# Kernel tuning notes

Hardware: AMD Instinct MI355X
Metric: run time of the kernel (lower is better)

Reference implementation:

```python
import jax, jax.numpy as jnp
import numpy as np

B = 256          # number of trees
DEPTH = 8        # complete binary tree depth -> 9 levels
M = 2 ** (DEPTH + 1) - 1   # 511 nodes per tree
N = B * M        # 130816 total nodes
X_SIZE = 128
H_SIZE = 128


def _build_forest():
    j = np.arange(M)
    parent_local = np.maximum((j - 1) // 2, 0)
    lvl = np.array([int(x + 1).bit_length() - 1 for x in j], dtype=np.int32)
    off = (np.arange(B) * M).astype(np.int32)
    parent = (parent_local[None, :] + off[:, None]).reshape(-1).astype(np.int32)
    level = np.tile(lvl, B)
    tree_id = np.repeat(np.arange(B, dtype=np.int32), M)
    isleaf = (level == DEPTH)
    jj = j[1:]
    edge_src = (jj[None, :] + off[:, None]).reshape(-1).astype(np.int32)   # child
    edge_dst = parent[edge_src]                                            # parent
    return parent, level, tree_id, isleaf, edge_src, edge_dst, off


def setup_inputs() -> dict:
    key = jax.random.key(0)
    ks = jax.random.split(key, 12)
    _, level, tree_id, isleaf, edge_src, edge_dst, root_ids = _build_forest()
    sx = 1.0 / np.sqrt(X_SIZE)
    sh = 1.0 / np.sqrt(H_SIZE)
    sxh = 1.0 / np.sqrt(X_SIZE + H_SIZE)
    inp = {
        "X": jax.random.normal(ks[0], (N, X_SIZE), dtype=jnp.float32),
        "h0": jnp.zeros((N, H_SIZE), jnp.float32),
        "c0": jnp.zeros((N, H_SIZE), jnp.float32),
        # bottom-up cell params
        "W_iou_bu": jax.random.normal(ks[1], (3 * H_SIZE, X_SIZE), dtype=jnp.float32) * sx,
        "U_iou_bu": jax.random.normal(ks[2], (3 * H_SIZE, H_SIZE), dtype=jnp.float32) * sh,
        "b_iou_bu": jnp.zeros((1, 3 * H_SIZE), jnp.float32),
        "Uf_bu": jax.random.normal(ks[3], (H_SIZE, H_SIZE), dtype=jnp.float32) * sh,
        "bf_bu": jax.random.normal(ks[4], (H_SIZE,), dtype=jnp.float32) * sh,
        # top-down cell params (x_size = X_SIZE + H_SIZE)
        "W_iou_td": jax.random.normal(ks[5], (3 * H_SIZE, X_SIZE + H_SIZE), dtype=jnp.float32) * sxh,
        "U_iou_td": jax.random.normal(ks[6], (3 * H_SIZE, H_SIZE), dtype=jnp.float32) * sh,
        "b_iou_td": jnp.zeros((1, 3 * H_SIZE), jnp.float32),
        "Uf_td": jax.random.normal(ks[7], (H_SIZE, H_SIZE), dtype=jnp.float32) * sh,
        "bf_td": jax.random.normal(ks[8], (H_SIZE,), dtype=jnp.float32) * sh,
        # graph structure
        "edge_src": jnp.asarray(edge_src),
        "edge_dst": jnp.asarray(edge_dst),
        "level": jnp.asarray(level),
        "tree_id": jnp.asarray(tree_id),
        "isleaf": jnp.asarray(isleaf),
        "root_ids": jnp.asarray(root_ids),
    }
    return inp


def _propagate(X_in, W_iou, U_iou, b_iou, Uf, bf, src, dst, level, no_in, h0, c0, order):
    """Level-synchronous ChildSum TreeLSTM propagation (== dgl.prop_nodes_topo)."""
    n = X_in.shape[0]
    WX = X_in @ W_iou.T                                   # [N, 3H]
    h, c = h0, c0
    for t in order:
        h_src = h[src]                                    # [E, H] gather child/parent states
        c_src = c[src]
        h_tild = jax.ops.segment_sum(h_src, dst, num_segments=n)
        f = jax.nn.sigmoid(h_src @ Uf.T + bf)             # per-edge forget gate
        c_red = jax.ops.segment_sum(f * c_src, dst, num_segments=n)
        iou = WX + h_tild @ U_iou.T + b_iou
        i, o, u = jnp.split(iou, 3, axis=1)
        c_base = jnp.where(no_in[:, None], c0, c_red)     # frontier nodes with no in-edges keep init c
        c_new = jax.nn.sigmoid(i) * jnp.tanh(u) + c_base
        h_new = jax.nn.sigmoid(o) * jnp.tanh(c_new)
        m = (level == t)[:, None]                          # only commit current topological level
        h = jnp.where(m, h_new, h)
        c = jnp.where(m, c_new, c)
    return h


def reference(X, h0, c0, W_iou_bu, U_iou_bu, b_iou_bu, Uf_bu, bf_bu,
              W_iou_td, U_iou_td, b_iou_td, Uf_td, bf_td,
              edge_src, edge_dst, level, tree_id, isleaf, root_ids):
    # bottom-up: messages flow child -> parent, leaves first
    h_bu = _propagate(X, W_iou_bu, U_iou_bu, b_iou_bu, Uf_bu, bf_bu,
                      edge_src, edge_dst, level, isleaf, h0, c0,
                      order=range(DEPTH, -1, -1))
    # top-down: reversed edges, root first
    X_td = jnp.concatenate([X, h_bu], axis=1)
    h_td = _propagate(X_td, W_iou_td, U_iou_td, b_iou_td, Uf_td, bf_td,
                      edge_dst, edge_src, level, level == 0, h0, c0,
                      order=range(0, DEPTH + 1))
    root_h_bottom_up = h_bu[root_ids]                     # [B, H]
    leaf = isleaf.astype(h_td.dtype)
    sums = jax.ops.segment_sum(h_td * leaf[:, None], tree_id, num_segments=root_ids.shape[0])
    cnt = jax.ops.segment_sum(leaf, tree_id, num_segments=root_ids.shape[0])
    leaves_h_top_down = sums / cnt[:, None]               # per-tree mean over leaves
    return jnp.concatenate([root_h_bottom_up, leaves_h_top_down], axis=1)
```

## Files before the change

### kernel.cpp

```cpp
#include <hip/hip_runtime.h>
#include <cmath>

#define NTREE 256
#define MPT 511
#define NNODE (NTREE * MPT)
#define HS 128

typedef __bf16 bf16x8 __attribute__((ext_vector_type(8)));
typedef float  f32x4  __attribute__((ext_vector_type(4)));

__device__ __forceinline__ float sigf(float x) {
  float e = __builtin_amdgcn_exp2f(x * -1.44269504f);
  return __builtin_amdgcn_rcpf(1.0f + e);
}
__device__ __forceinline__ float tanh_fast(float x) {
  float e = __builtin_amdgcn_exp2f(x * -2.88539008f);
  return __builtin_amdgcn_rcpf(1.0f + e) * 2.0f - 1.0f;
}
__device__ __forceinline__ f32x4 mm(bf16x8 a, bf16x8 b, f32x4 c) {
  return __builtin_amdgcn_mfma_f32_16x16x32_bf16(a, b, c, 0, 0, 0);
}
__device__ __forceinline__ int swz(int row, int rb, int kb) { return row * rb + (kb ^ ((row & 7) << 4)); }
__device__ __forceinline__ void st8(char* s, int row, int rb, int chunk, bf16x8 v) {
  *reinterpret_cast<bf16x8*>(s + swz(row, rb, chunk * 16)) = v;
}
__device__ __forceinline__ bf16x8 ld8(const char* s, int row, int rb, int kb) {
  return *reinterpret_cast<const bf16x8*>(s + swz(row, rb, kb));
}
__device__ __forceinline__ bf16x8 g8(const __bf16* p) { return *reinterpret_cast<const bf16x8*>(p); }
__device__ __forceinline__ bf16x8 gx8(const float* p) {
  float4 v0 = reinterpret_cast<const float4*>(p)[0];
  float4 v1 = reinterpret_cast<const float4*>(p)[1];
  bf16x8 o;
  o[0] = (__bf16)v0.x; o[1] = (__bf16)v0.y; o[2] = (__bf16)v0.z; o[3] = (__bf16)v0.w;
  o[4] = (__bf16)v1.x; o[5] = (__bf16)v1.y; o[6] = (__bf16)v1.z; o[7] = (__bf16)v1.w;
  return o;
}
__device__ __forceinline__ void stbf(char* s, int row, int rb, int kbyte, float v) {
  *reinterpret_cast<__bf16*>(s + row * rb + (kbyte ^ ((row & 7) << 4))) = (__bf16)v;
}

template <int MODE, bool EPI>
__global__ void __launch_bounds__(256, 2)
level_big(int t,
          const float*  __restrict__ Xf,
          const __bf16* __restrict__ W,
          const float*  __restrict__ bp,
          const __bf16* __restrict__ Uf,
          const float*  __restrict__ bf_,
          __bf16* __restrict__ h_bu,
          __bf16* __restrict__ h_td,
          float*  __restrict__ cws,
          float*  __restrict__ part)
{
  constexpr int KA = (MODE == 0) ? 128 : (MODE == 1) ? 256 : 384;
  constexpr int KS = KA / 32;
  constexpr int BK = (MODE == 3) ? 384 : 256;
  constexpr int RB = KA * 2;
  constexpr int HB = (MODE == 0) ? 0 : (MODE == 1) ? 256 : 512;
  constexpr bool LEAFOUT = (MODE == 3 && !EPI);

  __shared__ __align__(16) char sA[64 * RB];
  __shared__ int sG[64], sP[64];

  const int tid = threadIdx.x;
  const int w = tid >> 6, l = tid & 63, lr = l & 15, lk = l >> 4;

  if (tid < 64) {
    int v = blockIdx.x * 64 + tid;
    int b = v >> t;
    int j = (1 << t) - 1 + (v & ((1 << t) - 1));
    sG[tid] = b * MPT + j;
    sP[tid] = b * MPT + ((j - 1) >> 1);
  }
  __syncthreads();

#pragma unroll
  for (int it = 0; it < 4; ++it) {
    int idx = tid + it * 256, n = idx >> 4, e = idx & 15;
    st8(sA, n, RB, e, gx8(Xf + (size_t)sG[n] * HS + e * 8));
  }
  if constexpr (MODE >= 1) {
#pragma unroll
    for (int it = 0; it < 4; ++it) {
      int idx = tid + it * 256, n = idx >> 4, e = idx & 15;
      st8(sA, n, RB, 16 + e, g8(h_bu + (size_t)sG[n] * HS + e * 8));
    }
  }
  if constexpr (MODE == 3) {
#pragma unroll
    for (int it = 0; it < 4; ++it) {
      int idx = tid + it * 256, n = idx >> 4, e = idx & 15;
      st8(sA, n, RB, 32 + e, g8(h_td + (size_t)sP[n] * HS + e * 8));
    }
  }
  __syncthreads();

  float cb[2][4][4];
  float bia[2], boa[2], bua[2], bfa[2];
#pragma unroll
  for (int nf = 0; nf < 2; ++nf) {
    const int ch = w * 32 + nf * 16 + lr;
    bia[nf] = bp[ch]; boa[nf] = bp[ch + 128]; bua[nf] = bp[ch + 256];
    if constexpr (EPI) bfa[nf] = bf_[ch];
    if constexpr (MODE == 1 || MODE == 3) {
#pragma unroll
      for (int mf = 0; mf < 4; ++mf)
#pragma unroll
        for (int j = 0; j < 4; ++j) {
          const int nrow = 16 * mf + lk * 4 + j;
          const int src = (MODE == 1) ? sG[nrow] : sP[nrow];
          cb[nf][mf][j] = cws[(size_t)src * HS + ch];
        }
    }
  }

  f32x4 acc[6][4];
#pragma unroll
  for (int p = 0; p < 6; ++p)
#pragma unroll
    for (int mf = 0; mf < 4; ++mf) acc[p][mf] = 0.0f;

  bf16x8 A0[4], A1[4], Bb[3][6];
  auto ldA = [&](int ks, bf16x8* Ad) {
#pragma unroll
    for (int mf = 0; mf < 4; ++mf) Ad[mf] = ld8(sA, mf * 16 + lr, RB, ks * 64 + lk * 16);
  };
  auto ldB = [&](int ks, int s) {
#pragma unroll
    for (int g2 = 0; g2 < 3; ++g2)
#pragma unroll
      for (int nf = 0; nf < 2; ++nf)
        Bb[s][g2 * 2 + nf] = g8(W + (size_t)(g2 * 128 + w * 32 + nf * 16 + lr) * BK + ks * 32 + lk * 8);
  };

  ldB(0, 0); ldA(0, A0); ldB(1, 1);
#pragma unroll
  for (int ks = 0; ks < KS; ++ks) {
    bf16x8* Ac = (ks & 1) ? A1 : A0;
    bf16x8* An = (ks & 1) ? A0 : A1;
    if (ks + 1 < KS) ldA(ks + 1, An);
    if (ks + 2 < KS) ldB(ks + 2, (ks + 2) % 3);
#pragma unroll
    for (int p = 0; p < 6; ++p)
#pragma unroll
      for (int mf = 0; mf < 4; ++mf) acc[p][mf] = mm(Ac[mf], Bb[ks % 3][p], acc[p][mf]);
  }

  bf16x8 Uff[8];
  if constexpr (EPI) {
#pragma unroll
    for (int ks = 0; ks < 4; ++ks)
#pragma unroll
      for (int nf = 0; nf < 2; ++nf)
        Uff[ks * 2 + nf] = g8(Uf + (size_t)(w * 32 + nf * 16 + lr) * HS + ks * 32 + lk * 8);
  }

  __bf16* hp = (MODE == 3) ? h_td : h_bu;
  float cnv[2][4][4], hnv[2][4][4];
  float psum[2] = {0.0f, 0.0f};
#pragma unroll
  for (int nf = 0; nf < 2; ++nf) {
    const int ch = w * 32 + nf * 16 + lr;
#pragma unroll
    for (int mf = 0; mf < 4; ++mf)
#pragma unroll
      for (int j = 0; j < 4; ++j) {
        const int nrow = 16 * mf + lk * 4 + j;
        float cbase = (MODE == 0) ? 0.0f : cb[nf][mf][j];
        float cn = sigf(acc[nf][mf][j] + bia[nf]) * tanh_fast(acc[4 + nf][mf][j] + bua[nf]) + cbase;
        float hn = sigf(acc[2 + nf][mf][j] + boa[nf]) * tanh_fast(cn);
        if constexpr (!LEAFOUT) hp[(size_t)sG[nrow] * HS + ch] = (__bf16)hn;
        if constexpr (EPI) { cnv[nf][mf][j] = cn; hnv[nf][mf][j] = hn; }
        if constexpr (LEAFOUT) psum[nf] += hn;
      }
  }

  if constexpr (LEAFOUT) {
#pragma unroll
    for (int nf = 0; nf < 2; ++nf) {
      float s = psum[nf];
      s += __shfl_xor(s, 16);
      s += __shfl_xor(s, 32);
      if (lk == 0) part[(size_t)blockIdx.x * 128 + w * 32 + nf * 16 + lr] = s;
    }
  }

  if constexpr (EPI) {
    __syncthreads();
#pragma unroll
    for (int nf = 0; nf < 2; ++nf) {
      const int ch = w * 32 + nf * 16 + lr;
#pragma unroll
      for (int mf = 0; mf < 4; ++mf)
#pragma unroll
        for (int j = 0; j < 4; ++j)
          stbf(sA, 16 * mf + lk * 4 + j, RB, HB + 2 * ch, hnv[nf][mf][j]);
    }
    __syncthreads();
    f32x4 fa[4][2];
#pragma unroll
    for (int mf = 0; mf < 4; ++mf) { fa[mf][0] = 0.0f; fa[mf][1] = 0.0f; }
#pragma unroll
    for (int ks = 0; ks < 4; ++ks) {
      bf16x8 a0 = ld8(sA, lr,      RB, HB + ks * 64 + lk * 16);
      bf16x8 a1 = ld8(sA, 16 + lr, RB, HB + ks * 64 + lk * 16);
      bf16x8 a2 = ld8(sA, 32 + lr, RB, HB + ks * 64 + lk * 16);
      bf16x8 a3 = ld8(sA, 48 + lr, RB, HB + ks * 64 + lk * 16);
#pragma unroll
      for (int nf = 0; nf < 2; ++nf) {
        fa[0][nf] = mm(a0, Uff[ks * 2 + nf], fa[0][nf]);
        fa[1][nf] = mm(a1, Uff[ks * 2 + nf], fa[1][nf]);
        fa[2][nf] = mm(a2, Uff[ks * 2 + nf], fa[2][nf]);
        fa[3][nf] = mm(a3, Uff[ks * 2 + nf], fa[3][nf]);
      }
    }
#pragma unroll
    for (int nf = 0; nf < 2; ++nf) {
      const int ch = w * 32 + nf * 16 + lr;
      if constexpr (MODE == 3) {
#pragma unroll
        for (int mf = 0; mf < 4; ++mf)
#pragma unroll
          for (int j = 0; j < 4; ++j) {
            const int nrow = 16 * mf + lk * 4 + j;
            cws[(size_t)sG[nrow] * HS + ch] = sigf(fa[mf][nf][j] + bfa[nf]) * cnv[nf][mf][j];
          }
      } else {
#pragma unroll
        for (int mf = 0; mf < 4; ++mf)
#pragma unroll
          for (int p = 0; p < 2; ++p) {
            const int er = 16 * mf + lk * 4 + 2 * p;
            float f0 = sigf(fa[mf][nf][2 * p]     + bfa[nf]) * cnv[nf][mf][2 * p];
            float f1 = sigf(fa[mf][nf][2 * p + 1] + bfa[nf]) * cnv[nf][mf][2 * p + 1];
            const int gp = sP[er];
            cws[(size_t)gp * HS + ch] = f0 + f1;
            h_bu[(size_t)gp * HS + ch] = (__bf16)(hnv[nf][mf][2 * p] + hnv[nf][mf][2 * p + 1]);
          }
      }
    }
  }
}

__global__ void __launch_bounds__(512, 2)
small_both(const float* __restrict__ Xf,
           const __bf16* __restrict__ Wbu, const float* __restrict__ bbu,
           const __bf16* __restrict__ Ufb, const float* __restrict__ bfb,
           const __bf16* __restrict__ Wtd, const float* __restrict__ btd,
           const __bf16* __restrict__ Uft, const float* __restrict__ bft,
           __bf16* __restrict__ h_bu, __bf16* __restrict__ h_td,
           float* __restrict__ cws)
{
  __shared__ __align__(16) char sX[31 * 256];
  __shared__ __align__(16) char sH[31 * 256];
  __shared__ __align__(16) char sT[16 * 256];
  __shared__ __align__(16) char sTd[15 * 256];
  __shared__ float sCr[16][128];
  __shared__ float sFc[16][128];

  const int tid = threadIdx.x, w = tid >> 6, l = tid & 63, lr = l & 15, lk = l >> 4;
  const int ch = w * 16 + lr;
  const size_t base = (size_t)blockIdx.x * MPT * HS;

  for (int idx = tid; idx < 31 * 16; idx += 512) {
    int n = idx >> 4, e = idx & 15;
    st8(sX, n, 256, e, gx8(Xf + base + (size_t)n * HS + e * 8));
  }
  if (tid < 256) { int n = tid >> 4, e = tid & 15;
    st8(sT, n, 256, e, g8(h_bu + base + (size_t)(15 + n) * HS + e * 8)); }
  { int n = tid >> 5, e = tid & 31;
    reinterpret_cast<float4*>(&sCr[n][0])[e] =
        reinterpret_cast<const float4*>(cws + base + (size_t)(15 + n) * HS)[e]; }
  for (int idx = tid; idx < 15 * 16; idx += 512)
    *reinterpret_cast<float4*>(sTd + idx * 16) = float4{0.f, 0.f, 0.f, 0.f};

  {
    const float bia = bbu[ch], boa = bbu[ch + 128], bua = bbu[ch + 256], bfa = bfb[ch];
    bf16x8 Wb[8][3], Uff[4];
#pragma unroll
    for (int ks = 0; ks < 8; ++ks)
#pragma unroll
      for (int g2 = 0; g2 < 3; ++g2)
        Wb[ks][g2] = g8(Wbu + (size_t)(g2 * 128 + ch) * 256 + ks * 32 + lk * 8);
#pragma unroll
    for (int ks = 0; ks < 4; ++ks)
      Uff[ks] = g8(Ufb + (size_t)ch * HS + ks * 32 + lk * 8);
    __syncthreads();

    for (int t = 4; t >= 0; --t) {
      const int cnt = 1 << t, j0 = cnt - 1;
      f32x4 acc0 = 0.0f, acc1 = 0.0f, acc2 = 0.0f;
      bf16x8 Aa[3];
      auto ldA = [&](int ks, int s) {
        const int kb = (ks & 3) * 64 + lk * 16;
        Aa[s] = (ks < 4) ? ld8(sX, j0 + lr, 256, kb) : ld8(sT, lr, 256, kb);
      };
      ldA(0, 0); ldA(1, 1);
#pragma unroll
      for (int ks = 0; ks < 8; ++ks) {
        if (ks + 2 < 8) ldA(ks + 2, (ks + 2) % 3);
        acc0 = mm(Aa[ks % 3], Wb[ks][0], acc0);
        acc1 = mm(Aa[ks % 3], Wb[ks][1], acc1);
        acc2 = mm(Aa[ks % 3], Wb[ks][2], acc2);
      }
      float cnv[4], hnv[4];
#pragma unroll
      for (int j = 0; j < 4; ++j) {
        const int r = lk * 4 + j;
        float cn = sigf(acc0[j] + bia) * tanh_fast(acc2[j] + bua) + sCr[r][ch];
        float hn = sigf(acc1[j] + boa) * tanh_fast(cn);
        cnv[j] = cn; hnv[j] = hn;
        if (r < cnt) stbf(sH, j0 + r, 256, 2 * ch, hn);
      }
      if (t == 0 && lk == 0) h_bu[base + ch] = (__bf16)hnv[0];
      __syncthreads();
      if (t > 0) {
        f32x4 fa = 0.0f;
#pragma unroll
        for (int ks = 0; ks < 4; ++ks)
          fa = mm(ld8(sH, j0 + lr, 256, ks * 64 + lk * 16), Uff[ks], fa);
#pragma unroll
        for (int p = 0; p < 2; ++p) {
          const int pr = lk * 2 + p;
          if (pr < (cnt >> 1)) {
            float f0 = sigf(fa[2 * p]     + bfa) * cnv[2 * p];
            float f1 = sigf(fa[2 * p + 1] + bfa) * cnv[2 * p + 1];
            sCr[pr][ch] = f0 + f1;
            stbf(sT, pr, 256, 2 * ch, hnv[2 * p] + hnv[2 * p + 1]);
          }
        }
      }
      __syncthreads();
    }
  }

  {
    const float bia = btd[ch], boa = btd[ch + 128], bua = btd[ch + 256], bfa = bft[ch];
    bf16x8 Wt[12][3], Uff[4];
#pragma unroll
    for (int ks = 0; ks < 12; ++ks)
#pragma unroll
      for (int g2 = 0; g2 < 3; ++g2)
        Wt[ks][g2] = g8(Wtd + (size_t)(g2 * 128 + ch) * 384 + ks * 32 + lk * 8);
#pragma unroll
    for (int ks = 0; ks < 4; ++ks)
      Uff[ks] = g8(Uft + (size_t)ch * HS + ks * 32 + lk * 8);

    for (int t = 0; t <= 4; ++t) {
      const int cnt = 1 << t, j0 = cnt - 1;
      f32x4 acc0 = 0.0f, acc1 = 0.0f, acc2 = 0.0f;
      bf16x8 Aa[3];
      auto ldA = [&](int ks, int s) {
        const int kb = (ks & 3) * 64 + lk * 16;
        if (ks < 4)      Aa[s] = ld8(sX, j0 + lr, 256, kb);
        else if (ks < 8) Aa[s] = ld8(sH, j0 + lr, 256, kb);
        else { int pr = (j0 + lr - 1) >> 1; pr = pr < 0 ? 0 : pr;
               Aa[s] = ld8(sTd, pr, 256, kb); }
      };
      ldA(0, 0); ldA(1, 1);
#pragma unroll
      for (int ks = 0; ks < 12; ++ks) {
        if (ks + 2 < 12) ldA(ks + 2, (ks + 2) % 3);
        acc0 = mm(Aa[ks % 3], Wt[ks][0], acc0);
        acc1 = mm(Aa[ks % 3], Wt[ks][1], acc1);
        acc2 = mm(Aa[ks % 3], Wt[ks][2], acc2);
      }
      float cnv[4], hnv[4];
#pragma unroll
      for (int j = 0; j < 4; ++j) {
        const int r = lk * 4 + j;
        float cb = (t == 0) ? 0.0f : sFc[r >> 1][ch];
        float cn = sigf(acc0[j] + bia) * tanh_fast(acc2[j] + bua) + cb;
        float hn = sigf(acc1[j] + boa) * tanh_fast(cn);
        cnv[j] = cn; hnv[j] = hn;
        stbf(sT, r, 256, 2 * ch, hn);
        if (r < cnt && j0 + r < 15) stbf(sTd, j0 + r, 256, 2 * ch, hn);
        if (t == 4) h_td[base + (size_t)(15 + r) * HS + ch] = (__bf16)hn;
      }
      __syncthreads();
      f32x4 fa = 0.0f;
#pragma unroll
      for (int ks = 0; ks < 4; ++ks)
        fa = mm(ld8(sT, lr, 256, ks * 64 + lk * 16), Uff[ks], fa);
#pragma unroll
      for (int j = 0; j < 4; ++j) {
        const int r = lk * 4 + j;
        float fcv = sigf(fa[j] + bfa) * cnv[j];
        if (r < cnt) {
          if (t < 4) sFc[r][ch] = fcv;
          else       cws[base + (size_t)(15 + r) * HS + ch] = fcv;
        }
      }
      __syncthreads();
    }
  }
}

__global__ void __launch_bounds__(256)
prep(const float* __restrict__ Wbu, const float* __restrict__ Ubu,
     const float* __restrict__ Wtd, const float* __restrict__ Utd,
     const float* __restrict__ Ufb, const float* __restrict__ Uft,
     __bf16* wbu, __bf16* wtd, __bf16* ufb, __bf16* uft)
{
  int i = blockIdx.x * 256 + threadIdx.x;
  if (i < 98304) {
    int r = i >> 8, c = i & 255;
    wbu[i] = (__bf16)(c < 128 ? Wbu[r * 128 + c] : Ubu[r * 128 + c - 128]);
  } else if (i < 245760) {
    int k = i - 98304; int r = k / 384, c = k - r * 384;
    wtd[k] = (__bf16)(c < 256 ? Wtd[r * 256 + c] : Utd[r * 128 + (c - 256)]);
  } else if (i < 262144) {
    int k = i - 245760; ufb[k] = (__bf16)Ufb[k];
  } else {
    int k = i - 262144; uft[k] = (__bf16)Uft[k];
  }
}

__global__ void __launch_bounds__(128)
finalize_kernel(const __bf16* __restrict__ h_bu, const float* __restrict__ part,
                float* __restrict__ out)
{
  int b = blockIdx.x, ch = threadIdx.x;
  out[(size_t)b * 256 + ch] = (float)h_bu[((size_t)b * MPT) * HS + ch];
  const float* pp = part + (size_t)b * 512 + ch;
  out[(size_t)b * 256 + 128 + ch] = (pp[0] + pp[128] + pp[256] + pp[384]) * (1.0f / 256.0f);
}

extern "C" void kernel_launch(void* const* d_in, const int* in_sizes, int n_in,
                              void* d_out, int out_size, void* d_ws, size_t ws_size,
                              hipStream_t stream) {
  const float* X     = (const float*)d_in[0];
  const float* W_bu  = (const float*)d_in[3];
  const float* U_bu  = (const float*)d_in[4];
  const float* b_bu  = (const float*)d_in[5];
  const float* Uf_bu = (const float*)d_in[6];
  const float* bf_bu = (const float*)d_in[7];
  const float* W_td  = (const float*)d_in[8];
  const float* U_td  = (const float*)d_in[9];
  const float* b_td  = (const float*)d_in[10];
  const float* Uf_td = (const float*)d_in[11];
  const float* bf_td = (const float*)d_in[12];

  char* p = (char*)d_ws;
  __bf16* wbu  = (__bf16*)p; p += (size_t)384 * 256 * 2;
  __bf16* wtd  = (__bf16*)p; p += (size_t)384 * 384 * 2;
  __bf16* ufb  = (__bf16*)p; p += (size_t)128 * 128 * 2;
  __bf16* uft  = (__bf16*)p; p += (size_t)128 * 128 * 2;
  __bf16* h_bu = (__bf16*)p; p += (size_t)NNODE * HS * 2;
  __bf16* h_td = (__bf16*)p; p += (size_t)NNODE * HS * 2;
  float*  cws  = (float*)p;  p += (size_t)NNODE * HS * 4;
  float*  part = (float*)p;

  prep<<<1088, 256, 0, stream>>>(W_bu, U_bu, W_td, U_td, Uf_bu, Uf_td, wbu, wtd, ufb, uft);

  level_big<0, true><<<1024, 256, 0, stream>>>(8, X, wbu, b_bu, ufb, bf_bu, h_bu, h_td, cws, part);
  level_big<1, true><<<512,  256, 0, stream>>>(7, X, wbu, b_bu, ufb, bf_bu, h_bu, h_td, cws, part);
  level_big<1, true><<<256,  256, 0, stream>>>(6, X, wbu, b_bu, ufb, bf_bu, h_bu, h_td, cws, part);
  level_big<1, true><<<128,  256, 0, stream>>>(5, X, wbu, b_bu, ufb, bf_bu, h_bu, h_td, cws, part);

  small_both<<<256, 512, 0, stream>>>(X, wbu, b_bu, ufb, bf_bu,
                                      wtd, b_td, uft, bf_td, h_bu, h_td, cws);

  level_big<3, true ><<<128,  256, 0, stream>>>(5, X, wtd, b_td, uft, bf_td, h_bu, h_td, cws, part);
  level_big<3, true ><<<256,  256, 0, stream>>>(6, X, wtd, b_td, uft, bf_td, h_bu, h_td, cws, part);
  level_big<3, true ><<<512,  256, 0, stream>>>(7, X, wtd, b_td, uft, bf_td, h_bu, h_td, cws, part);
  level_big<3, false><<<1024, 256, 0, stream>>>(8, X, wtd, b_td, uft, bf_td, h_bu, h_td, cws, part);

  finalize_kernel<<<256, 128, 0, stream>>>(h_bu, part, (float*)d_out);
}
```

Baseline: 262.1 us.

## Add 512-thread leaf-level kernel with register-resident weights for the two leaf passes

Introduces level_big8, a 512-thread (8-wave) variant in which each wave owns 16 output channels and keeps its whole weight slice in registers, and uses it for the two largest launches, the bottom-up and top-down leaf levels. Splitting channels over twice as many waves reduces per-wave accumulator state and should give more latency hiding on the widest levels. The existing level_big kernel is simplified to cover only the interior modes. The cost is higher register pressure from the preloaded weights, and each block now loads the full weight slice up front.

```diff
diff --git a/kernel.cpp b/kernel.cpp
--- a/kernel.cpp
+++ b/kernel.cpp
@@ -41,6 +41,164 @@
 }
 
 template <int MODE, bool EPI>
+__global__ void __launch_bounds__(512, 2)
+level_big8(int t,
+           const float*  __restrict__ Xf,
+           const __bf16* __restrict__ W,
+           const float*  __restrict__ bp,
+           const __bf16* __restrict__ Uf,
+           const float*  __restrict__ bf_,
+           __bf16* __restrict__ h_bu,
+           __bf16* __restrict__ h_td,
+           float*  __restrict__ cws,
+           float*  __restrict__ part)
+{
+  constexpr int KA = (MODE == 0) ? 128 : 384;
+  constexpr int KS = KA / 32;
+  constexpr int BK = (MODE == 3) ? 384 : 256;
+  constexpr int RB = KA * 2;
+  constexpr int HB = (MODE == 0) ? 0 : 512;
+  constexpr bool LEAFOUT = (MODE == 3 && !EPI);
+
+  __shared__ __align__(16) char sA[64 * RB];
+  __shared__ int sG[64], sP[64];
+
+  const int tid = threadIdx.x;
+  const int w = tid >> 6, l = tid & 63, lr = l & 15, lk = l >> 4;
+  const int ch = w * 16 + lr;
+
+  if (tid < 64) {
+    int v = blockIdx.x * 64 + tid;
+    int b = v >> t;
+    int j = (1 << t) - 1 + (v & ((1 << t) - 1));
+    sG[tid] = b * MPT + j;
+    sP[tid] = b * MPT + ((j - 1) >> 1);
+  }
+  __syncthreads();
+
+  bf16x8 Wr[KS][3];
+#pragma unroll
+  for (int ks = 0; ks < KS; ++ks)
+#pragma unroll
+    for (int g2 = 0; g2 < 3; ++g2)
+      Wr[ks][g2] = g8(W + (size_t)(g2 * 128 + ch) * BK + ks * 32 + lk * 8);
+
+#pragma unroll
+  for (int it = 0; it < 2; ++it) {
+    int idx = tid + it * 512, n = idx >> 4, e = idx & 15;
+    st8(sA, n, RB, e, gx8(Xf + (size_t)sG[n] * HS + e * 8));
+  }
+  if constexpr (MODE == 3) {
+#pragma unroll
+    for (int it = 0; it < 2; ++it) {
+      int idx = tid + it * 512, n = idx >> 4, e = idx & 15;
+      st8(sA, n, RB, 16 + e, g8(h_bu + (size_t)sG[n] * HS + e * 8));
+    }
+#pragma unroll
+    for (int it = 0; it < 2; ++it) {
+      int idx = tid + it * 512, n = idx >> 4, e = idx & 15;
+      st8(sA, n, RB, 32 + e, g8(h_td + (size_t)sP[n] * HS + e * 8));
+    }
+  }
+  __syncthreads();
+
+  float cb[4][4];
+  const float bia = bp[ch], boa = bp[ch + 128], bua = bp[ch + 256];
+  float bfa = 0.0f;
+  if constexpr (EPI) bfa = bf_[ch];
+  if constexpr (MODE == 3) {
+#pragma unroll
+    for (int mf = 0; mf < 4; ++mf)
+#pragma unroll
+      for (int j = 0; j < 4; ++j)
+        cb[mf][j] = cws[(size_t)sP[16 * mf + lk * 4 + j] * HS + ch];
+  }
+
+  f32x4 acc[3][4];
+#pragma unroll
+  for (int g2 = 0; g2 < 3; ++g2)
+#pragma unroll
+    for (int mf = 0; mf < 4; ++mf) acc[g2][mf] = 0.0f;
+
+#pragma unroll
+  for (int ks = 0; ks < KS; ++ks) {
+    bf16x8 A0 = ld8(sA, lr,      RB, ks * 64 + lk * 16);
+    bf16x8 A1 = ld8(sA, 16 + lr, RB, ks * 64 + lk * 16);
+    bf16x8 A2 = ld8(sA, 32 + lr, RB, ks * 64 + lk * 16);
+    bf16x8 A3 = ld8(sA, 48 + lr, RB, ks * 64 + lk * 16);
+#pragma unroll
+    for (int g2 = 0; g2 < 3; ++g2) {
+      acc[g2][0] = mm(A0, Wr[ks][g2], acc[g2][0]);
+      acc[g2][1] = mm(A1, Wr[ks][g2], acc[g2][1]);
+      acc[g2][2] = mm(A2, Wr[ks][g2], acc[g2][2]);
+      acc[g2][3] = mm(A3, Wr[ks][g2], acc[g2][3]);
+    }
+  }
+
+  float cnv[4][4], hnv[4][4];
+  float psum = 0.0f;
+#pragma unroll
+  for (int mf = 0; mf < 4; ++mf)
+#pragma unroll
+    for (int j = 0; j < 4; ++j) {
+      const int nrow = 16 * mf + lk * 4 + j;
+      float cbase = (MODE == 0) ? 0.0f : cb[mf][j];
+      float cn = sigf(acc[0][mf][j] + bia) * tanh_fast(acc[2][mf][j] + bua) + cbase;
+      float hn = sigf(acc[1][mf][j] + boa) * tanh_fast(cn);
+      if constexpr (!LEAFOUT)
+        ((MODE == 3) ? h_td : h_bu)[(size_t)sG[nrow] * HS + ch] = (__bf16)hn;
+      if constexpr (EPI) { cnv[mf][j] = cn; hnv[mf][j] = hn; }
+      if constexpr (LEAFOUT) psum += hn;
+    }
+
+  if constexpr (LEAFOUT) {
+    float s = psum;
+    s += __shfl_xor(s, 16);
+    s += __shfl_xor(s, 32);
+    if (lk == 0) part[(size_t)blockIdx.x * 128 + ch] = s;
+  }
+
+  if constexpr (EPI) {
+    bf16x8 Uff[4];
+#pragma unroll
+    for (int ks = 0; ks < 4; ++ks)
+      Uff[ks] = g8(Uf + (size_t)ch * HS + ks * 32 + lk * 8);
+    __syncthreads();
+#pragma unroll
+    for (int mf = 0; mf < 4; ++mf)
+#pragma unroll
+      for (int j = 0; j < 4; ++j)
+        stbf(sA, 16 * mf + lk * 4 + j, RB, HB + 2 * ch, hnv[mf][j]);
+    __syncthreads();
+    f32x4 fa[4];
+#pragma unroll
+    for (int mf = 0; mf < 4; ++mf) fa[mf] = 0.0f;
+#pragma unroll
+    for (int ks = 0; ks < 4; ++ks) {
+      bf16x8 a0 = ld8(sA, lr,      RB, HB + ks * 64 + lk * 16);
+      bf16x8 a1 = ld8(sA, 16 + lr, RB, HB + ks * 64 + lk * 16);
+      bf16x8 a2 = ld8(sA, 32 + lr, RB, HB + ks * 64 + lk * 16);
+      bf16x8 a3 = ld8(sA, 48 + lr, RB, HB + ks * 64 + lk * 16);
+      fa[0] = mm(a0, Uff[ks], fa[0]);
+      fa[1] = mm(a1, Uff[ks], fa[1]);
+      fa[2] = mm(a2, Uff[ks], fa[2]);
+      fa[3] = mm(a3, Uff[ks], fa[3]);
+    }
+#pragma unroll
+    for (int mf = 0; mf < 4; ++mf)
+#pragma unroll
+      for (int p = 0; p < 2; ++p) {
+        const int er = 16 * mf + lk * 4 + 2 * p;
+        float f0 = sigf(fa[mf][2 * p]     + bfa) * cnv[mf][2 * p];
+        float f1 = sigf(fa[mf][2 * p + 1] + bfa) * cnv[mf][2 * p + 1];
+        const int gp = sP[er];
+        cws[(size_t)gp * HS + ch] = f0 + f1;
+        h_bu[(size_t)gp * HS + ch] = (__bf16)(hnv[mf][2 * p] + hnv[mf][2 * p + 1]);
+      }
+  }
+}
+
+template <int MODE>
 __global__ void __launch_bounds__(256, 2)
 level_big(int t,
           const float*  __restrict__ Xf,
@@ -50,15 +208,13 @@
           const float*  __restrict__ bf_,
           __bf16* __restrict__ h_bu,
           __bf16* __restrict__ h_td,
-          float*  __restrict__ cws,
-          float*  __restrict__ part)
+          float*  __restrict__ cws)
 {
-  constexpr int KA = (MODE == 0) ? 128 : (MODE == 1) ? 256 : 384;
+  constexpr int KA = (MODE == 1) ? 256 : 384;
   constexpr int KS = KA / 32;
   constexpr int BK = (MODE == 3) ? 384 : 256;
   constexpr int RB = KA * 2;
-  constexpr int HB = (MODE == 0) ? 0 : (MODE == 1) ? 256 : 512;
-  constexpr bool LEAFOUT = (MODE == 3 && !EPI);
+  constexpr int HB = (MODE == 1) ? 256 : 512;
 
   __shared__ __align__(16) char sA[64 * RB];
   __shared__ int sG[64], sP[64];
@@ -80,12 +236,10 @@
     int idx = tid + it * 256, n = idx >> 4, e = idx & 15;
     st8(sA, n, RB, e, gx8(Xf + (size_t)sG[n] * HS + e * 8));
   }
-  if constexpr (MODE >= 1) {
-#pragma unroll
-    for (int it = 0; it < 4; ++it) {
-      int idx = tid + it * 256, n = idx >> 4, e = idx & 15;
-      st8(sA, n, RB, 16 + e, g8(h_bu + (size_t)sG[n] * HS + e * 8));
-    }
+#pragma unroll
+  for (int it = 0; it < 4; ++it) {
+    int idx = tid + it * 256, n = idx >> 4, e = idx & 15;
+    st8(sA, n, RB, 16 + e, g8(h_bu + (size_t)sG[n] * HS + e * 8));
   }
   if constexpr (MODE == 3) {
 #pragma unroll
@@ -102,17 +256,15 @@
   for (int nf = 0; nf < 2; ++nf) {
     const int ch = w * 32 + nf * 16 + lr;
     bia[nf] = bp[ch]; boa[nf] = bp[ch + 128]; bua[nf] = bp[ch + 256];
-    if constexpr (EPI) bfa[nf] = bf_[ch];
-    if constexpr (MODE == 1 || MODE == 3) {
-#pragma unroll
-      for (int mf = 0; mf < 4; ++mf)
-#pragma unroll
-        for (int j = 0; j < 4; ++j) {
-          const int nrow = 16 * mf + lk * 4 + j;
-          const int src = (MODE == 1) ? sG[nrow] : sP[nrow];
-          cb[nf][mf][j] = cws[(size_t)src * HS + ch];
-        }
-    }
+    bfa[nf] = bf_[ch];
+#pragma unroll
+    for (int mf = 0; mf < 4; ++mf)
+#pragma unroll
+      for (int j = 0; j < 4; ++j) {
+        const int nrow = 16 * mf + lk * 4 + j;
+        const int src = (MODE == 1) ? sG[nrow] : sP[nrow];
+        cb[nf][mf][j] = cws[(size_t)src * HS + ch];
+      }
   }
 
   f32x4 acc[6][4];
@@ -148,17 +300,14 @@
   }
 
   bf16x8 Uff[8];
-  if constexpr (EPI) {
-#pragma unroll
-    for (int ks = 0; ks < 4; ++ks)
-#pragma unroll
-      for (int nf = 0; nf < 2; ++nf)
-        Uff[ks * 2 + nf] = g8(Uf + (size_t)(w * 32 + nf * 16 + lr) * HS + ks * 32 + lk * 8);
-  }
+#pragma unroll
+  for (int ks = 0; ks < 4; ++ks)
+#pragma unroll
+    for (int nf = 0; nf < 2; ++nf)
+      Uff[ks * 2 + nf] = g8(Uf + (size_t)(w * 32 + nf * 16 + lr) * HS + ks * 32 + lk * 8);
 
   __bf16* hp = (MODE == 3) ? h_td : h_bu;
   float cnv[2][4][4], hnv[2][4][4];
-  float psum[2] = {0.0f, 0.0f};
 #pragma unroll
   for (int nf = 0; nf < 2; ++nf) {
     const int ch = w * 32 + nf * 16 + lr;
@@ -167,78 +316,64 @@
 #pragma unroll
       for (int j = 0; j < 4; ++j) {
         const int nrow = 16 * mf + lk * 4 + j;
-        float cbase = (MODE == 0) ? 0.0f : cb[nf][mf][j];
-        float cn = sigf(acc[nf][mf][j] + bia[nf]) * tanh_fast(acc[4 + nf][mf][j] + bua[nf]) + cbase;
+        float cn = sigf(acc[nf][mf][j] + bia[nf]) * tanh_fast(acc[4 + nf][mf][j] + bua[nf]) + cb[nf][mf][j];
         float hn = sigf(acc[2 + nf][mf][j] + boa[nf]) * tanh_fast(cn);
-        if constexpr (!LEAFOUT) hp[(size_t)sG[nrow] * HS + ch] = (__bf16)hn;
-        if constexpr (EPI) { cnv[nf][mf][j] = cn; hnv[nf][mf][j] = hn; }
-        if constexpr (LEAFOUT) psum[nf] += hn;
-      }
-  }
-
-  if constexpr (LEAFOUT) {
+        hp[(size_t)sG[nrow] * HS + ch] = (__bf16)hn;
+        cnv[nf][mf][j] = cn; hnv[nf][mf][j] = hn;
+      }
+  }
+
+  __syncthreads();
+#pragma unroll
+  for (int nf = 0; nf < 2; ++nf) {
+    const int ch = w * 32 + nf * 16 + lr;
+#pragma unroll
+    for (int mf = 0; mf < 4; ++mf)
+#pragma unroll
+      for (int j = 0; j < 4; ++j)
+        stbf(sA, 16 * mf + lk * 4 + j, RB, HB + 2 * ch, hnv[nf][mf][j]);
+  }
+  __syncthreads();
+  f32x4 fa[4][2];
+#pragma unroll
+  for (int mf = 0; mf < 4; ++mf) { fa[mf][0] = 0.0f; fa[mf][1] = 0.0f; }
+#pragma unroll
+  for (int ks = 0; ks < 4; ++ks) {
+    bf16x8 a0 = ld8(sA, lr,      RB, HB + ks * 64 + lk * 16);
+    bf16x8 a1 = ld8(sA, 16 + lr, RB, HB + ks * 64 + lk * 16);
+    bf16x8 a2 = ld8(sA, 32 + lr, RB, HB + ks * 64 + lk * 16);
+    bf16x8 a3 = ld8(sA, 48 + lr, RB, HB + ks * 64 + lk * 16);
 #pragma unroll
     for (int nf = 0; nf < 2; ++nf) {
-      float s = psum[nf];
-      s += __shfl_xor(s, 16);
-      s += __shfl_xor(s, 32);
-      if (lk == 0) part[(size_t)blockIdx.x * 128 + w * 32 + nf * 16 + lr] = s;
-    }
-  }
-
-  if constexpr (EPI) {
-    __syncthreads();
-#pragma unroll
-    for (int nf = 0; nf < 2; ++nf) {
-      const int ch = w * 32 + nf * 16 + lr;
+      fa[0][nf] = mm(a0, Uff[ks * 2 + nf], fa[0][nf]);
+      fa[1][nf] = mm(a1, Uff[ks * 2 + nf], fa[1][nf]);
+      fa[2][nf] = mm(a2, Uff[ks * 2 + nf], fa[2][nf]);
+      fa[3][nf] = mm(a3, Uff[ks * 2 + nf], fa[3][nf]);
+    }
+  }
+#pragma unroll
+  for (int nf = 0; nf < 2; ++nf) {
+    const int ch = w * 32 + nf * 16 + lr;
+    if constexpr (MODE == 3) {
 #pragma unroll
       for (int mf = 0; mf < 4; ++mf)
 #pragma unroll
-        for (int j = 0; j < 4; ++j)
-          stbf(sA, 16 * mf + lk * 4 + j, RB, HB + 2 * ch, hnv[nf][mf][j]);
-    }
-    __syncthreads();
-    f32x4 fa[4][2];
-#pragma unroll
-    for (int mf = 0; mf < 4; ++mf) { fa[mf][0] = 0.0f; fa[mf][1] = 0.0f; }
-#pragma unroll
-    for (int ks = 0; ks < 4; ++ks) {
-      bf16x8 a0 = ld8(sA, lr,      RB, HB + ks * 64 + lk * 16);
-      bf16x8 a1 = ld8(sA, 16 + lr, RB, HB + ks * 64 + lk * 16);
-      bf16x8 a2 = ld8(sA, 32 + lr, RB, HB + ks * 64 + lk * 16);
-      bf16x8 a3 = ld8(sA, 48 + lr, RB, HB + ks * 64 + lk * 16);
-#pragma unroll
-      for (int nf = 0; nf < 2; ++nf) {
-        fa[0][nf] = mm(a0, Uff[ks * 2 + nf], fa[0][nf]);
-        fa[1][nf] = mm(a1, Uff[ks * 2 + nf], fa[1][nf]);
-        fa[2][nf] = mm(a2, Uff[ks * 2 + nf], fa[2][nf]);
-        fa[3][nf] = mm(a3, Uff[ks * 2 + nf], fa[3][nf]);
-      }
-    }
-#pragma unroll
-    for (int nf = 0; nf < 2; ++nf) {
-      const int ch = w * 32 + nf * 16 + lr;
-      if constexpr (MODE == 3) {
-#pragma unroll
-        for (int mf = 0; mf < 4; ++mf)
-#pragma unroll
-          for (int j = 0; j < 4; ++j) {
-            const int nrow = 16 * mf + lk * 4 + j;
-            cws[(size_t)sG[nrow] * HS + ch] = sigf(fa[mf][nf][j] + bfa[nf]) * cnv[nf][mf][j];
-          }
-      } else {
-#pragma unroll
-        for (int mf = 0; mf < 4; ++mf)
-#pragma unroll
-          for (int p = 0; p < 2; ++p) {
-            const int er = 16 * mf + lk * 4 + 2 * p;
-            float f0 = sigf(fa[mf][nf][2 * p]     + bfa[nf]) * cnv[nf][mf][2 * p];
-            float f1 = sigf(fa[mf][nf][2 * p + 1] + bfa[nf]) * cnv[nf][mf][2 * p + 1];
-            const int gp = sP[er];
-            cws[(size_t)gp * HS + ch] = f0 + f1;
-            h_bu[(size_t)gp * HS + ch] = (__bf16)(hnv[nf][mf][2 * p] + hnv[nf][mf][2 * p + 1]);
-          }
-      }
+        for (int j = 0; j < 4; ++j) {
+          const int nrow = 16 * mf + lk * 4 + j;
+          cws[(size_t)sG[nrow] * HS + ch] = sigf(fa[mf][nf][j] + bfa[nf]) * cnv[nf][mf][j];
+        }
+    } else {
+#pragma unroll
+      for (int mf = 0; mf < 4; ++mf)
+#pragma unroll
+        for (int p = 0; p < 2; ++p) {
+          const int er = 16 * mf + lk * 4 + 2 * p;
+          float f0 = sigf(fa[mf][nf][2 * p]     + bfa[nf]) * cnv[nf][mf][2 * p];
+          float f1 = sigf(fa[mf][nf][2 * p + 1] + bfa[nf]) * cnv[nf][mf][2 * p + 1];
+          const int gp = sP[er];
+          cws[(size_t)gp * HS + ch] = f0 + f1;
+          h_bu[(size_t)gp * HS + ch] = (__bf16)(hnv[nf][mf][2 * p] + hnv[nf][mf][2 * p + 1]);
+        }
     }
   }
 }
@@ -370,8 +505,8 @@
 #pragma unroll
       for (int j = 0; j < 4; ++j) {
         const int r = lk * 4 + j;
-        float cb = (t == 0) ? 0.0f : sFc[r >> 1][ch];
-        float cn = sigf(acc0[j] + bia) * tanh_fast(acc2[j] + bua) + cb;
+        float cbv = (t == 0) ? 0.0f : sFc[r >> 1][ch];
+        float cn = sigf(acc0[j] + bia) * tanh_fast(acc2[j] + bua) + cbv;
         float hn = sigf(acc1[j] + boa) * tanh_fast(cn);
         cnv[j] = cn; hnv[j] = hn;
         stbf(sT, r, 256, 2 * ch, hn);
@@ -454,18 +589,18 @@
 
   prep<<<1088, 256, 0, stream>>>(W_bu, U_bu, W_td, U_td, Uf_bu, Uf_td, wbu, wtd, ufb, uft);
 
-  level_big<0, true><<<1024, 256, 0, stream>>>(8, X, wbu, b_bu, ufb, bf_bu, h_bu, h_td, cws, part);
-  level_big<1, true><<<512,  256, 0, stream>>>(7, X, wbu, b_bu, ufb, bf_bu, h_bu, h_td, cws, part);
-  level_big<1, true><<<256,  256, 0, stream>>>(6, X, wbu, b_bu, ufb, bf_bu, h_bu, h_td, cws, part);
-  level_big<1, true><<<128,  256, 0, stream>>>(5, X, wbu, b_bu, ufb, bf_bu, h_bu, h_td, cws, part);
+  level_big8<0, true><<<1024, 512, 0, stream>>>(8, X, wbu, b_bu, ufb, bf_bu, h_bu, h_td, cws, part);
+  level_big<1><<<512, 256, 0, stream>>>(7, X, wbu, b_bu, ufb, bf_bu, h_bu, h_td, cws);
+  level_big<1><<<256, 256, 0, stream>>>(6, X, wbu, b_bu, ufb, bf_bu, h_bu, h_td, cws);
+  level_big<1><<<128, 256, 0, stream>>>(5, X, wbu, b_bu, ufb, bf_bu, h_bu, h_td, cws);
 
   small_both<<<256, 512, 0, stream>>>(X, wbu, b_bu, ufb, bf_bu,
                                       wtd, b_td, uft, bf_td, h_bu, h_td, cws);
 
-  level_big<3, true ><<<128,  256, 0, stream>>>(5, X, wtd, b_td, uft, bf_td, h_bu, h_td, cws, part);
-  level_big<3, true ><<<256,  256, 0, stream>>>(6, X, wtd, b_td, uft, bf_td, h_bu, h_td, cws, part);
-  level_big<3, true ><<<512,  256, 0, stream>>>(7, X, wtd, b_td, uft, bf_td, h_bu, h_td, cws, part);
-  level_big<3, false><<<1024, 256, 0, stream>>>(8, X, wtd, b_td, uft, bf_td, h_bu, h_td, cws, part);
+  level_big<3><<<128, 256, 0, stream>>>(5, X, wtd, b_td, uft, bf_td, h_bu, h_td, cws);
+  level_big<3><<<256, 256, 0, stream>>>(6, X, wtd, b_td, uft, bf_td, h_bu, h_td, cws);
+  level_big<3><<<512, 256, 0, stream>>>(7, X, wtd, b_td, uft, bf_td, h_bu, h_td, cws);
+  level_big8<3, false><<<1024, 512, 0, stream>>>(8, X, wtd, b_td, uft, bf_td, h_bu, h_td, cws, part);
 
   finalize_kernel<<<256, 128, 0, stream>>>(h_bu, part, (float*)d_out);
 }
```

After: 262.7 us. Within noise of the previous version (+0.2%).
